# Kernel optimization log

Hardware: AMD Instinct MI355X
Metric: run time of the kernel (lower is better)

Reference implementation:

```python
import jax, jax.numpy as jnp
import numpy as np

HEADS = 4
DIM_HEAD = 64
QUERY_DIM = 512
CONTEXT_DIM = 512
INNER = HEADS * DIM_HEAD  # 256
SCALE = DIM_HEAD ** -0.5


def setup_inputs() -> dict:
    key = jax.random.key(0)
    ks = jax.random.split(key, 9)
    b, n, m = 4, 2048, 2048
    inp = {
        'x1': jax.random.normal(ks[0], (b, n, QUERY_DIM), jnp.float32),
        'x2': jax.random.normal(ks[1], (b, n, QUERY_DIM), jnp.float32),
        'context': jax.random.normal(ks[2], (b, m, CONTEXT_DIM), jnp.float32),
        # weights stored [in, out] (= torch weight.T)
        'Wq': jax.random.normal(ks[3], (QUERY_DIM, INNER), jnp.float32) * (QUERY_DIM ** -0.5),
        'Wq2': jax.random.normal(ks[4], (QUERY_DIM, INNER), jnp.float32) * (QUERY_DIM ** -0.5),
        'Wk': jax.random.normal(ks[5], (CONTEXT_DIM, INNER), jnp.float32) * (CONTEXT_DIM ** -0.5),
        'Wv': jax.random.normal(ks[6], (CONTEXT_DIM, INNER), jnp.float32) * (CONTEXT_DIM ** -0.5),
        'Wo': jax.random.normal(ks[7], (INNER, QUERY_DIM), jnp.float32) * (INNER ** -0.5),
        'bo': jax.random.normal(ks[8], (QUERY_DIM,), jnp.float32) * 0.01,
    }
    return inp


def _split_heads(t):
    # [b, n, h*d] -> [b, h, n, d]
    b, n, _ = t.shape
    return t.reshape(b, n, HEADS, DIM_HEAD).transpose(0, 2, 1, 3)


def reference(x1, x2, context, Wq, Wq2, Wk, Wv, Wo, bo):
    q = _split_heads(x1 @ Wq)
    q2 = _split_heads(x2 @ Wq2)
    k = _split_heads(context @ Wk)
    v = _split_heads(context @ Wv)
    sim = jnp.einsum('bhid,bhjd->bhij', q, k) * SCALE
    sim2 = jnp.einsum('bhid,bhjd->bhij', q2, k) * SCALE
    attn = 0.3 * jax.nn.softmax(sim, axis=-1) + 0.7 * jax.nn.softmax(sim2, axis=-1)
    out = jnp.einsum('bhij,bhjd->bhid', attn, v)  # [b, h, n, d]
    b, h, n, d = out.shape
    out = out.transpose(0, 2, 1, 3).reshape(b, n, h * d)
    return out @ Wo + bo
```

## Files before the change

kernel.cpp:

```cpp
#include <hip/hip_runtime.h>

typedef __attribute__((ext_vector_type(8))) short bf16x8;
typedef __attribute__((ext_vector_type(4))) float f32x4;
typedef unsigned short ushort_t;
typedef unsigned int uint_t;

__device__ __forceinline__ ushort_t f2bf(float f) {
    return __builtin_bit_cast(ushort_t, (__bf16)f);
}
__device__ __forceinline__ uint_t pack2(float a, float b) {
    return (uint_t)f2bf(a) | ((uint_t)f2bf(b) << 16);
}

#define LOG2E 1.4426950408889634f

#define WT_OFF   0
#define WOT_OFF  524288
#define QKV_OFF  655360
#define QKV_SZ   2097152
#define QKV_OFF_Z3 (3 * (size_t)QKV_SZ)
#define O_OFF    9043968

__global__ __launch_bounds__(256) void transpose_w(
    const float* __restrict__ Wq, const float* __restrict__ Wq2,
    const float* __restrict__ Wk, const float* __restrict__ Wv,
    const float* __restrict__ Wo, ushort_t* __restrict__ ws)
{
    __shared__ ushort_t lT[64][72];
    const int j = blockIdx.y;
    const int bx = blockIdx.x;
    const float* in;
    ushort_t* out;
    int C;
    if (j < 4) {
        in = (j == 0) ? Wq : (j == 1) ? Wq2 : (j == 2) ? Wk : Wv;
        out = ws + WT_OFF + (size_t)j * 131072; C = 256;
    } else {
        in = Wo; out = ws + WOT_OFF; C = 512;
    }
    const int R = 131072 / C;
    const int tc = C >> 6;
    const int r0 = (bx / tc) * 64, c0 = (bx % tc) * 64;
    const int t = threadIdx.x;
    const int ir = t >> 4, ic = (t & 15) * 4;
#pragma unroll
    for (int i = 0; i < 4; ++i) {
        const int r = ir + i * 16;
        float4 v = *(const float4*)(in + (size_t)(r0 + r) * C + c0 + ic);
        uint2 w; w.x = pack2(v.x, v.y); w.y = pack2(v.z, v.w);
        *(uint2*)&lT[r][ic] = w;
    }
    __syncthreads();
    const int oc = t >> 2, rr0 = (t & 3) * 16;
    ushort_t g[16];
#pragma unroll
    for (int k = 0; k < 16; ++k) g[k] = lT[rr0 + k][oc];
    ushort_t* op = out + (size_t)(c0 + oc) * R + r0 + rr0;
    *(uint4*)op = *(const uint4*)&g[0];
    *(uint4*)(op + 8) = *(const uint4*)&g[8];
}

#define PROJ_STAGE(K0, BUF) do {                                                     \
    _Pragma("unroll")                                                                \
    for (int it_ = 0; it_ < 4; ++it_) {                                              \
        const int p_ = tid + it_ * 256;                                              \
        const ushort_t* bp_ = Bt + (size_t)(p_ >> 2) * 512 + (K0) + ((p_ & 3) << 3); \
        __builtin_amdgcn_global_load_lds(                                            \
            (const __attribute__((address_space(1))) void*)bp_,                      \
            (__attribute__((address_space(3))) void*)&lB[BUF][p_ * 8], 16, 0, 0);    \
    }                                                                                \
} while (0)

__global__ __launch_bounds__(256) void proj_gemm(
    const float* __restrict__ x1, const float* __restrict__ x2,
    const float* __restrict__ ctx, const ushort_t* __restrict__ Wt,
    ushort_t* __restrict__ QKV)
{
    __shared__ __align__(16) ushort_t lB[2][256 * 32];
    const int z = blockIdx.y;
    const float* A = (z == 0) ? x1 : (z == 1) ? x2 : ctx;
    const ushort_t* Bt = Wt + (size_t)z * 131072;
    const float sc = (z < 2) ? (0.125f * LOG2E) : 1.0f;
    const int tid = threadIdx.x;
    const int wave = tid >> 6, lane = tid & 63;
    const int quad = lane >> 4, l16 = lane & 15;
    const size_t row0 = (size_t)blockIdx.x * 64;

    PROJ_STAGE(0, 0);

    const float* arow = A + (row0 + wave * 16 + l16) * 512 + quad * 8;
    float4 a0 = *(const float4*)(arow);
    float4 a1 = *(const float4*)(arow + 4);

    f32x4 acc[16] = {};
    for (int k0 = 0; k0 < 512; k0 += 32) {
        const int pb = (k0 >> 5) & 1;
        __syncthreads();
        if (k0 + 32 < 512) PROJ_STAGE(k0 + 32, 1 - pb);
        float4 n0 = a0, n1 = a1;
        if (k0 + 32 < 512) {
            n0 = *(const float4*)(arow + k0 + 32);
            n1 = *(const float4*)(arow + k0 + 36);
        }
        uint4 aw;
        aw.x = pack2(a0.x, a0.y); aw.y = pack2(a0.z, a0.w);
        aw.z = pack2(a1.x, a1.y); aw.w = pack2(a1.z, a1.w);
        bf16x8 af = __builtin_bit_cast(bf16x8, aw);
#pragma unroll
        for (int c = 0; c < 16; ++c) {
            bf16x8 bfr = *(const bf16x8*)&lB[pb][(c * 16 + l16) * 32 + quad * 8];
            acc[c] = __builtin_amdgcn_mfma_f32_16x16x32_bf16(af, bfr, acc[c], 0, 0, 0);
        }
        a0 = n0; a1 = n1;
    }

    if (z == 3) {
        const int b = (int)(row0 >> 11);
        const int tokl = ((int)row0 & 2047) + wave * 16 + quad * 4;
        ushort_t* Vt = QKV + QKV_OFF_Z3;
#pragma unroll
        for (int c = 0; c < 16; ++c) {
            const int col = c * 16 + l16;
            const int h = col >> 6, d = col & 63;
            uint2 w;
            w.x = pack2(acc[c][0], acc[c][1]);
            w.y = pack2(acc[c][2], acc[c][3]);
            *(uint2*)(Vt + ((size_t)((b * 4 + h) * 64 + d)) * 2048 + tokl) = w;
        }
    } else {
        ushort_t* C = QKV + (size_t)z * QKV_SZ;
#pragma unroll
        for (int c = 0; c < 16; ++c) {
            const int col = c * 16 + l16;
#pragma unroll
            for (int r = 0; r < 4; ++r)
                C[(row0 + wave * 16 + quad * 4 + r) * 256 + col] = f2bf(acc[c][r] * sc);
        }
    }
}

#define OUT_STAGE(K0, BUF) do {                                                      \
    _Pragma("unroll")                                                                \
    for (int it_ = 0; it_ < 2; ++it_) {                                              \
        const int p_ = tid + it_ * 256;                                              \
        const ushort_t* bp_ = Wot + (size_t)(col0 + (p_ >> 2)) * 256 + (K0) + ((p_ & 3) << 3); \
        __builtin_amdgcn_global_load_lds(                                            \
            (const __attribute__((address_space(1))) void*)bp_,                      \
            (__attribute__((address_space(3))) void*)&lB[BUF][p_ * 8], 16, 0, 0);    \
    }                                                                                \
} while (0)

__global__ __launch_bounds__(256) void out_gemm(
    const ushort_t* __restrict__ Op, const ushort_t* __restrict__ Wot,
    const float* __restrict__ bias, float* __restrict__ out)
{
    __shared__ __align__(16) ushort_t lB[2][128 * 32];
    const int tid = threadIdx.x;
    const int wave = tid >> 6, lane = tid & 63;
    const int quad = lane >> 4, l16 = lane & 15;
    const size_t row0 = (size_t)blockIdx.x * 64;
    const int col0 = blockIdx.y * 128;

    OUT_STAGE(0, 0);
    const ushort_t* arow = Op + (row0 + wave * 16 + l16) * 256 + quad * 8;
    bf16x8 af = *(const bf16x8*)(arow);

    f32x4 acc[8] = {};
    for (int k0 = 0; k0 < 256; k0 += 32) {
        const int pb = (k0 >> 5) & 1;
        __syncthreads();
        if (k0 + 32 < 256) OUT_STAGE(k0 + 32, 1 - pb);
        bf16x8 an = af;
        if (k0 + 32 < 256) an = *(const bf16x8*)(arow + k0 + 32);
#pragma unroll
        for (int c = 0; c < 8; ++c) {
            bf16x8 bfr = *(const bf16x8*)&lB[pb][(c * 16 + l16) * 32 + quad * 8];
            acc[c] = __builtin_amdgcn_mfma_f32_16x16x32_bf16(af, bfr, acc[c], 0, 0, 0);
        }
        af = an;
    }
#pragma unroll
    for (int c = 0; c < 8; ++c) {
        const int col = col0 + c * 16 + l16;
        const float bv = bias[col];
#pragma unroll
        for (int r = 0; r < 4; ++r)
            out[(row0 + wave * 16 + quad * 4 + r) * 512 + col] = acc[c][r] + bv;
    }
}


#define ATTN_STAGE(MB, KDST, VDST) do {                                                 \
    _Pragma("unroll")                                                                   \
    for (int it_ = 0; it_ < 2; ++it_) {                                                 \
        const int cc_ = tid + it_ * 256;                                                \
        const int g_ = (cc_ ^ (cc_ >> 3)) & 7;                                          \
        const ushort_t* kp_ = Kb + (size_t)(tok0 + (MB) + (cc_ >> 3)) * 256 + in0 + g_ * 8; \
        __builtin_amdgcn_global_load_lds(                                               \
            (const __attribute__((address_space(1))) void*)kp_,                         \
            (__attribute__((address_space(3))) void*)&(KDST)[cc_ * 8], 16, 0, 0);       \
        const ushort_t* vp_ = Vt + (size_t)(bh64 + (cc_ >> 3)) * 2048 + (MB) + g_ * 8;  \
        __builtin_amdgcn_global_load_lds(                                               \
            (const __attribute__((address_space(1))) void*)vp_,                         \
            (__attribute__((address_space(3))) void*)&(VDST)[cc_ * 8], 16, 0, 0);       \
    }                                                                                   \
} while (0)

__global__ __launch_bounds__(256) void attn_fused(
    const ushort_t* __restrict__ Qb, const ushort_t* __restrict__ Q2b,
    const ushort_t* __restrict__ Kb, const ushort_t* __restrict__ Vt,
    ushort_t* __restrict__ Ob)
{
    __shared__ __align__(16) ushort_t lK[3][64 * 64];
    __shared__ __align__(16) ushort_t lV[3][64 * 64];
    __shared__ __align__(16) ushort_t lP[4][2][16 * 72];

    const int qt = blockIdx.x;
    const int bh = blockIdx.y;
    const int tid = threadIdx.x;
    const int wave = tid >> 6, lane = tid & 63;
    const int quad = lane >> 4, l16 = lane & 15;
    const int l7 = l16 & 7;
    const size_t tok0 = (size_t)(bh >> 2) * 2048;
    const int in0 = (bh & 3) * 64;
    const int bh64 = bh * 64;
    ushort_t* lPw0 = &lP[wave][0][0];
    ushort_t* lPw1 = &lP[wave][1][0];

    bf16x8 q1f[2], q2f[2];
    {
        const ushort_t* qr1 = Qb  + (tok0 + qt * 64 + wave * 16 + l16) * 256 + in0;
        const ushort_t* qr2 = Q2b + (tok0 + qt * 64 + wave * 16 + l16) * 256 + in0;
#pragma unroll
        for (int ks = 0; ks < 2; ++ks) {
            q1f[ks] = *(const bf16x8*)(qr1 + ks * 32 + quad * 8);
            q2f[ks] = *(const bf16x8*)(qr2 + ks * 32 + quad * 8);
        }
    }

    ushort_t* pKcur = &lK[0][0]; ushort_t* pVcur = &lV[0][0];
    ushort_t* pKpre = &lK[1][0]; ushort_t* pVpre = &lV[1][0];
    ushort_t* pKold = &lK[2][0]; ushort_t* pVold = &lV[2][0];

    ATTN_STAGE(0, pKcur, pVcur);

    f32x4 o1[4] = {}, o2[4] = {};
    bf16x8 pa1[2], pa2[2];
    float l1 = 0.f, l2 = 0.f;

    for (int i = 0; i < 32; ++i) {
        __syncthreads();
        if (i < 31) ATTN_STAGE((i + 1) * 64, pKpre, pVpre);

        f32x4 st1[4] = {}, st2[4] = {};
#pragma unroll
        for (int c = 0; c < 4; ++c) {
#pragma unroll
            for (int ks = 0; ks < 2; ++ks) {
                bf16x8 kf = *(const bf16x8*)&pKcur[(c * 16 + l16) * 64 +
                                                   ((((ks * 4 + quad) ^ l7) & 7) << 3)];
                st1[c] = __builtin_amdgcn_mfma_f32_16x16x32_bf16(kf, q1f[ks], st1[c], 0, 0, 0);
                st2[c] = __builtin_amdgcn_mfma_f32_16x16x32_bf16(kf, q2f[ks], st2[c], 0, 0, 0);
            }
        }

        if (i > 0) {
#pragma unroll
            for (int c = 0; c < 4; ++c) {
#pragma unroll
                for (int ks = 0; ks < 2; ++ks) {
                    bf16x8 vf = *(const bf16x8*)&pVold[(c * 16 + l16) * 64 +
                                                       ((((ks * 4 + quad) ^ l7) & 7) << 3)];
                    o1[c] = __builtin_amdgcn_mfma_f32_16x16x32_bf16(vf, pa1[ks], o1[c], 0, 0, 0);
                    o2[c] = __builtin_amdgcn_mfma_f32_16x16x32_bf16(vf, pa2[ks], o2[c], 0, 0, 0);
                }
            }
        }

#pragma unroll
        for (int c = 0; c < 4; ++c) {
            float p0 = __builtin_amdgcn_exp2f(st1[c][0]);
            float p1 = __builtin_amdgcn_exp2f(st1[c][1]);
            float p2 = __builtin_amdgcn_exp2f(st1[c][2]);
            float p3 = __builtin_amdgcn_exp2f(st1[c][3]);
            l1 += (p0 + p1) + (p2 + p3);
            uint2 w; w.x = pack2(p0, p1); w.y = pack2(p2, p3);
            *(uint2*)&lPw0[l16 * 72 + c * 16 + quad * 4] = w;
            float r0 = __builtin_amdgcn_exp2f(st2[c][0]);
            float r1 = __builtin_amdgcn_exp2f(st2[c][1]);
            float r2 = __builtin_amdgcn_exp2f(st2[c][2]);
            float r3 = __builtin_amdgcn_exp2f(st2[c][3]);
            l2 += (r0 + r1) + (r2 + r3);
            uint2 y; y.x = pack2(r0, r1); y.y = pack2(r2, r3);
            *(uint2*)&lPw1[l16 * 72 + c * 16 + quad * 4] = y;
        }
#pragma unroll
        for (int ks = 0; ks < 2; ++ks) {
            pa1[ks] = *(const bf16x8*)&lPw0[l16 * 72 + ks * 32 + quad * 8];
            pa2[ks] = *(const bf16x8*)&lPw1[l16 * 72 + ks * 32 + quad * 8];
        }

        ushort_t* tK = pKold; pKold = pKcur; pKcur = pKpre; pKpre = tK;
        ushort_t* tV = pVold; pVold = pVcur; pVcur = pVpre; pVpre = tV;
    }

#pragma unroll
    for (int c = 0; c < 4; ++c) {
#pragma unroll
        for (int ks = 0; ks < 2; ++ks) {
            bf16x8 vf = *(const bf16x8*)&pVold[(c * 16 + l16) * 64 +
                                               ((((ks * 4 + quad) ^ l7) & 7) << 3)];
            o1[c] = __builtin_amdgcn_mfma_f32_16x16x32_bf16(vf, pa1[ks], o1[c], 0, 0, 0);
            o2[c] = __builtin_amdgcn_mfma_f32_16x16x32_bf16(vf, pa2[ks], o2[c], 0, 0, 0);
        }
    }

    l1 += __shfl_xor(l1, 16, 64); l1 += __shfl_xor(l1, 32, 64);
    l2 += __shfl_xor(l2, 16, 64); l2 += __shfl_xor(l2, 32, 64);
    const float inv1 = 0.3f / l1, inv2 = 0.7f / l2;

    ushort_t* orow = Ob + (tok0 + qt * 64 + wave * 16 + l16) * 256 + in0;
#pragma unroll
    for (int c = 0; c < 4; ++c) {
        const float f0 = o1[c][0] * inv1 + o2[c][0] * inv2;
        const float f1 = o1[c][1] * inv1 + o2[c][1] * inv2;
        const float f2 = o1[c][2] * inv1 + o2[c][2] * inv2;
        const float f3 = o1[c][3] * inv1 + o2[c][3] * inv2;
        uint2 w; w.x = pack2(f0, f1); w.y = pack2(f2, f3);
        *(uint2*)(orow + c * 16 + quad * 4) = w;
    }
}

extern "C" void kernel_launch(void* const* d_in, const int* in_sizes, int n_in,
                              void* d_out, int out_size, void* d_ws, size_t ws_size,
                              hipStream_t stream)
{
    (void)in_sizes; (void)n_in; (void)out_size; (void)ws_size;
    const float* x1  = (const float*)d_in[0];
    const float* x2  = (const float*)d_in[1];
    const float* ctx = (const float*)d_in[2];
    const float* Wq  = (const float*)d_in[3];
    const float* Wq2 = (const float*)d_in[4];
    const float* Wk  = (const float*)d_in[5];
    const float* Wv  = (const float*)d_in[6];
    const float* Wo  = (const float*)d_in[7];
    const float* bo  = (const float*)d_in[8];
    ushort_t* ws  = (ushort_t*)d_ws;
    float* out = (float*)d_out;

    ushort_t* Wt  = ws + WT_OFF;
    ushort_t* Wot = ws + WOT_OFF;
    ushort_t* QKV = ws + QKV_OFF;
    ushort_t* Q   = QKV;
    ushort_t* Q2  = QKV + 1 * (size_t)QKV_SZ;
    ushort_t* Kp  = QKV + 2 * (size_t)QKV_SZ;
    ushort_t* Vt  = QKV + 3 * (size_t)QKV_SZ;
    ushort_t* Op  = ws + O_OFF;

    transpose_w<<<dim3(32, 5),  256, 0, stream>>>(Wq, Wq2, Wk, Wv, Wo, ws);
    proj_gemm  <<<dim3(128, 4), 256, 0, stream>>>(x1, x2, ctx, Wt, QKV);
    attn_fused <<<dim3(32, 16), 256, 0, stream>>>(Q, Q2, Kp, Vt, Op);
    out_gemm   <<<dim3(128, 4), 256, 0, stream>>>(Op, Wot, bo, out);
}
```

Measured before the change: 176.0 us.

## Process two query sub-tiles per wave in attention to reuse K/V fragments

Attention blocks shrink from 4 waves to 2, and each wave now handles 32 query rows as two 16-row groups. K and V fragments read from LDS are loaded once and used for both groups, which halves the LDS read traffic per MFMA. The K/V staging loop is adjusted so 128 threads fill the same tiles. In exchange, each wave holds roughly twice as many accumulator and fragment registers, which may lower occupancy, and there are fewer waves per block to hide latency.

```diff
diff --git a/kernel.cpp b/kernel.cpp
--- a/kernel.cpp
+++ b/kernel.cpp
@@ -192,8 +192,8 @@
 
 #define ATTN_STAGE(MB, KDST, VDST) do {                                                 \
     _Pragma("unroll")                                                                   \
-    for (int it_ = 0; it_ < 2; ++it_) {                                                 \
-        const int cc_ = tid + it_ * 256;                                                \
+    for (int it_ = 0; it_ < 4; ++it_) {                                                 \
+        const int cc_ = tid + it_ * 128;                                                \
         const int g_ = (cc_ ^ (cc_ >> 3)) & 7;                                          \
         const ushort_t* kp_ = Kb + (size_t)(tok0 + (MB) + (cc_ >> 3)) * 256 + in0 + g_ * 8; \
         __builtin_amdgcn_global_load_lds(                                               \
@@ -206,14 +206,47 @@
     }                                                                                   \
 } while (0)
 
-__global__ __launch_bounds__(256) void attn_fused(
+#define QK_SM(QG, PW0, PW1) do {                                                        \
+    f32x4 st1[4] = {}, st2[4] = {};                                                     \
+    _Pragma("unroll")                                                                   \
+    for (int c = 0; c < 4; ++c) {                                                       \
+        _Pragma("unroll")                                                               \
+        for (int ks = 0; ks < 2; ++ks) {                                                \
+            st1[c] = __builtin_amdgcn_mfma_f32_16x16x32_bf16(kf[c][ks], q1f[QG][ks], st1[c], 0, 0, 0); \
+            st2[c] = __builtin_amdgcn_mfma_f32_16x16x32_bf16(kf[c][ks], q2f[QG][ks], st2[c], 0, 0, 0); \
+        } }                                                                             \
+    _Pragma("unroll")                                                                   \
+    for (int c = 0; c < 4; ++c) {                                                       \
+        float p0 = __builtin_amdgcn_exp2f(st1[c][0]);                                   \
+        float p1 = __builtin_amdgcn_exp2f(st1[c][1]);                                   \
+        float p2 = __builtin_amdgcn_exp2f(st1[c][2]);                                   \
+        float p3 = __builtin_amdgcn_exp2f(st1[c][3]);                                   \
+        l1[QG] += (p0 + p1) + (p2 + p3);                                                \
+        uint2 w; w.x = pack2(p0, p1); w.y = pack2(p2, p3);                              \
+        *(uint2*)&(PW0)[l16 * 72 + c * 16 + quad * 4] = w;                              \
+        float r0 = __builtin_amdgcn_exp2f(st2[c][0]);                                   \
+        float r1 = __builtin_amdgcn_exp2f(st2[c][1]);                                   \
+        float r2 = __builtin_amdgcn_exp2f(st2[c][2]);                                   \
+        float r3 = __builtin_amdgcn_exp2f(st2[c][3]);                                   \
+        l2[QG] += (r0 + r1) + (r2 + r3);                                                \
+        uint2 y; y.x = pack2(r0, r1); y.y = pack2(r2, r3);                              \
+        *(uint2*)&(PW1)[l16 * 72 + c * 16 + quad * 4] = y;                              \
+    }                                                                                   \
+    _Pragma("unroll")                                                                   \
+    for (int ks = 0; ks < 2; ++ks) {                                                    \
+        pa1[QG][ks] = *(const bf16x8*)&(PW0)[l16 * 72 + ks * 32 + quad * 8];            \
+        pa2[QG][ks] = *(const bf16x8*)&(PW1)[l16 * 72 + ks * 32 + quad * 8];            \
+    }                                                                                   \
+} while (0)
+
+__global__ __launch_bounds__(128) void attn_fused(
     const ushort_t* __restrict__ Qb, const ushort_t* __restrict__ Q2b,
     const ushort_t* __restrict__ Kb, const ushort_t* __restrict__ Vt,
     ushort_t* __restrict__ Ob)
 {
     __shared__ __align__(16) ushort_t lK[3][64 * 64];
     __shared__ __align__(16) ushort_t lV[3][64 * 64];
-    __shared__ __align__(16) ushort_t lP[4][2][16 * 72];
+    __shared__ __align__(16) ushort_t lP[2][2][2][16 * 72];
 
     const int qt = blockIdx.x;
     const int bh = blockIdx.y;
@@ -224,17 +257,20 @@
     const size_t tok0 = (size_t)(bh >> 2) * 2048;
     const int in0 = (bh & 3) * 64;
     const int bh64 = bh * 64;
-    ushort_t* lPw0 = &lP[wave][0][0];
-    ushort_t* lPw1 = &lP[wave][1][0];
-
-    bf16x8 q1f[2], q2f[2];
-    {
-        const ushort_t* qr1 = Qb  + (tok0 + qt * 64 + wave * 16 + l16) * 256 + in0;
-        const ushort_t* qr2 = Q2b + (tok0 + qt * 64 + wave * 16 + l16) * 256 + in0;
+    ushort_t* lPw00 = &lP[wave][0][0][0];
+    ushort_t* lPw01 = &lP[wave][0][1][0];
+    ushort_t* lPw10 = &lP[wave][1][0][0];
+    ushort_t* lPw11 = &lP[wave][1][1][0];
+
+    bf16x8 q1f[2][2], q2f[2][2];
+#pragma unroll
+    for (int qg = 0; qg < 2; ++qg) {
+        const ushort_t* qr1 = Qb  + (tok0 + qt * 64 + wave * 32 + qg * 16 + l16) * 256 + in0;
+        const ushort_t* qr2 = Q2b + (tok0 + qt * 64 + wave * 32 + qg * 16 + l16) * 256 + in0;
 #pragma unroll
         for (int ks = 0; ks < 2; ++ks) {
-            q1f[ks] = *(const bf16x8*)(qr1 + ks * 32 + quad * 8);
-            q2f[ks] = *(const bf16x8*)(qr2 + ks * 32 + quad * 8);
+            q1f[qg][ks] = *(const bf16x8*)(qr1 + ks * 32 + quad * 8);
+            q2f[qg][ks] = *(const bf16x8*)(qr2 + ks * 32 + quad * 8);
         }
     }
 
@@ -244,26 +280,14 @@
 
     ATTN_STAGE(0, pKcur, pVcur);
 
-    f32x4 o1[4] = {}, o2[4] = {};
-    bf16x8 pa1[2], pa2[2];
-    float l1 = 0.f, l2 = 0.f;
+    f32x4 o1[2][4] = {}, o2[2][4] = {};
+    bf16x8 pa1[2][2], pa2[2][2];
+    float l1[2] = {0.f, 0.f}, l2[2] = {0.f, 0.f};
 
     for (int i = 0; i < 32; ++i) {
         __syncthreads();
         if (i < 31) ATTN_STAGE((i + 1) * 64, pKpre, pVpre);
 
-        f32x4 st1[4] = {}, st2[4] = {};
-#pragma unroll
-        for (int c = 0; c < 4; ++c) {
-#pragma unroll
-            for (int ks = 0; ks < 2; ++ks) {
-                bf16x8 kf = *(const bf16x8*)&pKcur[(c * 16 + l16) * 64 +
-                                                   ((((ks * 4 + quad) ^ l7) & 7) << 3)];
-                st1[c] = __builtin_amdgcn_mfma_f32_16x16x32_bf16(kf, q1f[ks], st1[c], 0, 0, 0);
-                st2[c] = __builtin_amdgcn_mfma_f32_16x16x32_bf16(kf, q2f[ks], st2[c], 0, 0, 0);
-            }
-        }
-
         if (i > 0) {
 #pragma unroll
             for (int c = 0; c < 4; ++c) {
@@ -271,34 +295,24 @@
                 for (int ks = 0; ks < 2; ++ks) {
                     bf16x8 vf = *(const bf16x8*)&pVold[(c * 16 + l16) * 64 +
                                                        ((((ks * 4 + quad) ^ l7) & 7) << 3)];
-                    o1[c] = __builtin_amdgcn_mfma_f32_16x16x32_bf16(vf, pa1[ks], o1[c], 0, 0, 0);
-                    o2[c] = __builtin_amdgcn_mfma_f32_16x16x32_bf16(vf, pa2[ks], o2[c], 0, 0, 0);
+                    o1[0][c] = __builtin_amdgcn_mfma_f32_16x16x32_bf16(vf, pa1[0][ks], o1[0][c], 0, 0, 0);
+                    o1[1][c] = __builtin_amdgcn_mfma_f32_16x16x32_bf16(vf, pa1[1][ks], o1[1][c], 0, 0, 0);
+                    o2[0][c] = __builtin_amdgcn_mfma_f32_16x16x32_bf16(vf, pa2[0][ks], o2[0][c], 0, 0, 0);
+                    o2[1][c] = __builtin_amdgcn_mfma_f32_16x16x32_bf16(vf, pa2[1][ks], o2[1][c], 0, 0, 0);
                 }
             }
         }
 
-#pragma unroll
-        for (int c = 0; c < 4; ++c) {
-            float p0 = __builtin_amdgcn_exp2f(st1[c][0]);
-            float p1 = __builtin_amdgcn_exp2f(st1[c][1]);
-            float p2 = __builtin_amdgcn_exp2f(st1[c][2]);
-            float p3 = __builtin_amdgcn_exp2f(st1[c][3]);
-            l1 += (p0 + p1) + (p2 + p3);
-            uint2 w; w.x = pack2(p0, p1); w.y = pack2(p2, p3);
-            *(uint2*)&lPw0[l16 * 72 + c * 16 + quad * 4] = w;
-            float r0 = __builtin_amdgcn_exp2f(st2[c][0]);
-            float r1 = __builtin_amdgcn_exp2f(st2[c][1]);
-            float r2 = __builtin_amdgcn_exp2f(st2[c][2]);
-            float r3 = __builtin_amdgcn_exp2f(st2[c][3]);
-            l2 += (r0 + r1) + (r2 + r3);
-            uint2 y; y.x = pack2(r0, r1); y.y = pack2(r2, r3);
-            *(uint2*)&lPw1[l16 * 72 + c * 16 + quad * 4] = y;
-        }
-#pragma unroll
-        for (int ks = 0; ks < 2; ++ks) {
-            pa1[ks] = *(const bf16x8*)&lPw0[l16 * 72 + ks * 32 + quad * 8];
-            pa2[ks] = *(const bf16x8*)&lPw1[l16 * 72 + ks * 32 + quad * 8];
-        }
+        bf16x8 kf[4][2];
+#pragma unroll
+        for (int c = 0; c < 4; ++c)
+#pragma unroll
+            for (int ks = 0; ks < 2; ++ks)
+                kf[c][ks] = *(const bf16x8*)&pKcur[(c * 16 + l16) * 64 +
+                                                   ((((ks * 4 + quad) ^ l7) & 7) << 3)];
+
+        QK_SM(0, lPw00, lPw01);
+        QK_SM(1, lPw10, lPw11);
 
         ushort_t* tK = pKold; pKold = pKcur; pKcur = pKpre; pKpre = tK;
         ushort_t* tV = pVold; pVold = pVcur; pVcur = pVpre; pVpre = tV;
@@ -310,24 +324,29 @@
         for (int ks = 0; ks < 2; ++ks) {
             bf16x8 vf = *(const bf16x8*)&pVold[(c * 16 + l16) * 64 +
                                                ((((ks * 4 + quad) ^ l7) & 7) << 3)];
-            o1[c] = __builtin_amdgcn_mfma_f32_16x16x32_bf16(vf, pa1[ks], o1[c], 0, 0, 0);
-            o2[c] = __builtin_amdgcn_mfma_f32_16x16x32_bf16(vf, pa2[ks], o2[c], 0, 0, 0);
-        }
-    }
-
-    l1 += __shfl_xor(l1, 16, 64); l1 += __shfl_xor(l1, 32, 64);
-    l2 += __shfl_xor(l2, 16, 64); l2 += __shfl_xor(l2, 32, 64);
-    const float inv1 = 0.3f / l1, inv2 = 0.7f / l2;
-
-    ushort_t* orow = Ob + (tok0 + qt * 64 + wave * 16 + l16) * 256 + in0;
-#pragma unroll
-    for (int c = 0; c < 4; ++c) {
-        const float f0 = o1[c][0] * inv1 + o2[c][0] * inv2;
-        const float f1 = o1[c][1] * inv1 + o2[c][1] * inv2;
-        const float f2 = o1[c][2] * inv1 + o2[c][2] * inv2;
-        const float f3 = o1[c][3] * inv1 + o2[c][3] * inv2;
-        uint2 w; w.x = pack2(f0, f1); w.y = pack2(f2, f3);
-        *(uint2*)(orow + c * 16 + quad * 4) = w;
+            o1[0][c] = __builtin_amdgcn_mfma_f32_16x16x32_bf16(vf, pa1[0][ks], o1[0][c], 0, 0, 0);
+            o1[1][c] = __builtin_amdgcn_mfma_f32_16x16x32_bf16(vf, pa1[1][ks], o1[1][c], 0, 0, 0);
+            o2[0][c] = __builtin_amdgcn_mfma_f32_16x16x32_bf16(vf, pa2[0][ks], o2[0][c], 0, 0, 0);
+            o2[1][c] = __builtin_amdgcn_mfma_f32_16x16x32_bf16(vf, pa2[1][ks], o2[1][c], 0, 0, 0);
+        }
+    }
+
+#pragma unroll
+    for (int qg = 0; qg < 2; ++qg) {
+        float L1 = l1[qg], L2 = l2[qg];
+        L1 += __shfl_xor(L1, 16, 64); L1 += __shfl_xor(L1, 32, 64);
+        L2 += __shfl_xor(L2, 16, 64); L2 += __shfl_xor(L2, 32, 64);
+        const float inv1 = 0.3f / L1, inv2 = 0.7f / L2;
+        ushort_t* orow = Ob + (tok0 + qt * 64 + wave * 32 + qg * 16 + l16) * 256 + in0;
+#pragma unroll
+        for (int c = 0; c < 4; ++c) {
+            const float f0 = o1[qg][c][0] * inv1 + o2[qg][c][0] * inv2;
+            const float f1 = o1[qg][c][1] * inv1 + o2[qg][c][1] * inv2;
+            const float f2 = o1[qg][c][2] * inv1 + o2[qg][c][2] * inv2;
+            const float f3 = o1[qg][c][3] * inv1 + o2[qg][c][3] * inv2;
+            uint2 w; w.x = pack2(f0, f1); w.y = pack2(f2, f3);
+            *(uint2*)(orow + c * 16 + quad * 4) = w;
+        }
     }
 }
 
@@ -359,6 +378,6 @@
 
     transpose_w<<<dim3(32, 5),  256, 0, stream>>>(Wq, Wq2, Wk, Wv, Wo, ws);
     proj_gemm  <<<dim3(128, 4), 256, 0, stream>>>(x1, x2, ctx, Wt, QKV);
-    attn_fused <<<dim3(32, 16), 256, 0, stream>>>(Q, Q2, Kp, Vt, Op);
+    attn_fused <<<dim3(32, 16), 128, 0, stream>>>(Q, Q2, Kp, Vt, Op);
     out_gemm   <<<dim3(128, 4), 256, 0, stream>>>(Op, Wot, bo, out);
 }
```

Measured after the change: 188.9 us. +7.3%, slower.

## Double K-tile depth to 64 with XOR-swizzled LDS in projection and output GEMMs

Applied to the files above, without the earlier changes.

The projection and output GEMMs now stage 64-wide K slices of the weight matrix per iteration instead of 32. This halves the number of barriers and loop trips, and the LDS layout is XOR-swizzled across 16-byte chunks to avoid bank conflicts on the wider rows. The cost is twice the LDS per block, which may lower occupancy, plus more register pressure from prefetching extra A fragments.

```diff
diff --git a/kernel.cpp b/kernel.cpp
--- a/kernel.cpp
+++ b/kernel.cpp
@@ -62,12 +62,13 @@
 
 #define PROJ_STAGE(K0, BUF) do {                                                     \
     _Pragma("unroll")                                                                \
-    for (int it_ = 0; it_ < 4; ++it_) {                                              \
-        const int p_ = tid + it_ * 256;                                              \
-        const ushort_t* bp_ = Bt + (size_t)(p_ >> 2) * 512 + (K0) + ((p_ & 3) << 3); \
+    for (int it_ = 0; it_ < 8; ++it_) {                                              \
+        const int cc_ = tid + it_ * 256;                                             \
+        const int g_ = (cc_ ^ (cc_ >> 3)) & 7;                                       \
+        const ushort_t* bp_ = Bt + (size_t)(cc_ >> 3) * 512 + (K0) + g_ * 8;         \
         __builtin_amdgcn_global_load_lds(                                            \
             (const __attribute__((address_space(1))) void*)bp_,                      \
-            (__attribute__((address_space(3))) void*)&lB[BUF][p_ * 8], 16, 0, 0);    \
+            (__attribute__((address_space(3))) void*)&lB[BUF][cc_ * 8], 16, 0, 0);   \
     }                                                                                \
 } while (0)
 
@@ -76,7 +77,7 @@
     const float* __restrict__ ctx, const ushort_t* __restrict__ Wt,
     ushort_t* __restrict__ QKV)
 {
-    __shared__ __align__(16) ushort_t lB[2][256 * 32];
+    __shared__ __align__(16) ushort_t lB[2][256 * 64];
     const int z = blockIdx.y;
     const float* A = (z == 0) ? x1 : (z == 1) ? x2 : ctx;
     const ushort_t* Bt = Wt + (size_t)z * 131072;
@@ -84,34 +85,50 @@
     const int tid = threadIdx.x;
     const int wave = tid >> 6, lane = tid & 63;
     const int quad = lane >> 4, l16 = lane & 15;
+    const int l7 = l16 & 7;
     const size_t row0 = (size_t)blockIdx.x * 64;
 
     PROJ_STAGE(0, 0);
 
     const float* arow = A + (row0 + wave * 16 + l16) * 512 + quad * 8;
-    float4 a0 = *(const float4*)(arow);
-    float4 a1 = *(const float4*)(arow + 4);
+    float4 a[4];
+    a[0] = *(const float4*)(arow);
+    a[1] = *(const float4*)(arow + 4);
+    a[2] = *(const float4*)(arow + 32);
+    a[3] = *(const float4*)(arow + 36);
 
     f32x4 acc[16] = {};
-    for (int k0 = 0; k0 < 512; k0 += 32) {
-        const int pb = (k0 >> 5) & 1;
+    for (int k0 = 0; k0 < 512; k0 += 64) {
+        const int pb = (k0 >> 6) & 1;
         __syncthreads();
-        if (k0 + 32 < 512) PROJ_STAGE(k0 + 32, 1 - pb);
-        float4 n0 = a0, n1 = a1;
-        if (k0 + 32 < 512) {
-            n0 = *(const float4*)(arow + k0 + 32);
-            n1 = *(const float4*)(arow + k0 + 36);
-        }
-        uint4 aw;
-        aw.x = pack2(a0.x, a0.y); aw.y = pack2(a0.z, a0.w);
-        aw.z = pack2(a1.x, a1.y); aw.w = pack2(a1.z, a1.w);
-        bf16x8 af = __builtin_bit_cast(bf16x8, aw);
+        if (k0 + 64 < 512) PROJ_STAGE(k0 + 64, 1 - pb);
+        float4 n[4] = {a[0], a[1], a[2], a[3]};
+        if (k0 + 64 < 512) {
+            n[0] = *(const float4*)(arow + k0 + 64);
+            n[1] = *(const float4*)(arow + k0 + 68);
+            n[2] = *(const float4*)(arow + k0 + 96);
+            n[3] = *(const float4*)(arow + k0 + 100);
+        }
+        bf16x8 af[2];
+#pragma unroll
+        for (int ks = 0; ks < 2; ++ks) {
+            uint4 aw;
+            aw.x = pack2(a[2 * ks].x, a[2 * ks].y);
+            aw.y = pack2(a[2 * ks].z, a[2 * ks].w);
+            aw.z = pack2(a[2 * ks + 1].x, a[2 * ks + 1].y);
+            aw.w = pack2(a[2 * ks + 1].z, a[2 * ks + 1].w);
+            af[ks] = __builtin_bit_cast(bf16x8, aw);
+        }
 #pragma unroll
         for (int c = 0; c < 16; ++c) {
-            bf16x8 bfr = *(const bf16x8*)&lB[pb][(c * 16 + l16) * 32 + quad * 8];
-            acc[c] = __builtin_amdgcn_mfma_f32_16x16x32_bf16(af, bfr, acc[c], 0, 0, 0);
-        }
-        a0 = n0; a1 = n1;
+#pragma unroll
+            for (int ks = 0; ks < 2; ++ks) {
+                bf16x8 bfr = *(const bf16x8*)&lB[pb][(c * 16 + l16) * 64 +
+                                                     (((ks * 4 + quad) ^ l7) << 3)];
+                acc[c] = __builtin_amdgcn_mfma_f32_16x16x32_bf16(af[ks], bfr, acc[c], 0, 0, 0);
+            }
+        }
+        a[0] = n[0]; a[1] = n[1]; a[2] = n[2]; a[3] = n[3];
     }
 
     if (z == 3) {
@@ -141,12 +158,13 @@
 
 #define OUT_STAGE(K0, BUF) do {                                                      \
     _Pragma("unroll")                                                                \
-    for (int it_ = 0; it_ < 2; ++it_) {                                              \
-        const int p_ = tid + it_ * 256;                                              \
-        const ushort_t* bp_ = Wot + (size_t)(col0 + (p_ >> 2)) * 256 + (K0) + ((p_ & 3) << 3); \
+    for (int it_ = 0; it_ < 4; ++it_) {                                              \
+        const int cc_ = tid + it_ * 256;                                             \
+        const int g_ = (cc_ ^ (cc_ >> 3)) & 7;                                       \
+        const ushort_t* bp_ = Wot + (size_t)(col0 + (cc_ >> 3)) * 256 + (K0) + g_ * 8; \
         __builtin_amdgcn_global_load_lds(                                            \
             (const __attribute__((address_space(1))) void*)bp_,                      \
-            (__attribute__((address_space(3))) void*)&lB[BUF][p_ * 8], 16, 0, 0);    \
+            (__attribute__((address_space(3))) void*)&lB[BUF][cc_ * 8], 16, 0, 0);   \
     }                                                                                \
 } while (0)
 
@@ -154,30 +172,37 @@
     const ushort_t* __restrict__ Op, const ushort_t* __restrict__ Wot,
     const float* __restrict__ bias, float* __restrict__ out)
 {
-    __shared__ __align__(16) ushort_t lB[2][128 * 32];
+    __shared__ __align__(16) ushort_t lB[2][128 * 64];
     const int tid = threadIdx.x;
     const int wave = tid >> 6, lane = tid & 63;
     const int quad = lane >> 4, l16 = lane & 15;
+    const int l7 = l16 & 7;
     const size_t row0 = (size_t)blockIdx.x * 64;
     const int col0 = blockIdx.y * 128;
 
     OUT_STAGE(0, 0);
     const ushort_t* arow = Op + (row0 + wave * 16 + l16) * 256 + quad * 8;
-    bf16x8 af = *(const bf16x8*)(arow);
+    bf16x8 af0 = *(const bf16x8*)(arow);
+    bf16x8 af1 = *(const bf16x8*)(arow + 32);
 
     f32x4 acc[8] = {};
-    for (int k0 = 0; k0 < 256; k0 += 32) {
-        const int pb = (k0 >> 5) & 1;
+    for (int k0 = 0; k0 < 256; k0 += 64) {
+        const int pb = (k0 >> 6) & 1;
         __syncthreads();
-        if (k0 + 32 < 256) OUT_STAGE(k0 + 32, 1 - pb);
-        bf16x8 an = af;
-        if (k0 + 32 < 256) an = *(const bf16x8*)(arow + k0 + 32);
+        if (k0 + 64 < 256) OUT_STAGE(k0 + 64, 1 - pb);
+        bf16x8 an0 = af0, an1 = af1;
+        if (k0 + 64 < 256) {
+            an0 = *(const bf16x8*)(arow + k0 + 64);
+            an1 = *(const bf16x8*)(arow + k0 + 96);
+        }
 #pragma unroll
         for (int c = 0; c < 8; ++c) {
-            bf16x8 bfr = *(const bf16x8*)&lB[pb][(c * 16 + l16) * 32 + quad * 8];
-            acc[c] = __builtin_amdgcn_mfma_f32_16x16x32_bf16(af, bfr, acc[c], 0, 0, 0);
-        }
-        af = an;
+            bf16x8 b0 = *(const bf16x8*)&lB[pb][(c * 16 + l16) * 64 + ((quad ^ l7) << 3)];
+            acc[c] = __builtin_amdgcn_mfma_f32_16x16x32_bf16(af0, b0, acc[c], 0, 0, 0);
+            bf16x8 b1 = *(const bf16x8*)&lB[pb][(c * 16 + l16) * 64 + (((4 + quad) ^ l7) << 3)];
+            acc[c] = __builtin_amdgcn_mfma_f32_16x16x32_bf16(af1, b1, acc[c], 0, 0, 0);
+        }
+        af0 = an0; af1 = an1;
     }
 #pragma unroll
     for (int c = 0; c < 8; ++c) {
```

Measured after the change: 170.1 us. -3.4%, faster.
